# Optimization experiments

Measured on AMD Instinct MI355X. Metric: run time of the kernel, lower is better.

The kernel has to match this reference:

```python
import jax, jax.numpy as jnp
import numpy as np

D_MODEL = 2048
NUM_HEADS = 16
D_K = D_MODEL // NUM_HEADS
B, S, PAST = 2, 1024, 3072


def setup_inputs() -> dict:
    key = jax.random.key(0)
    ks = jax.random.split(key, 12)
    s = 1.0 / np.sqrt(D_MODEL)
    inp = {
        "x": jax.random.normal(ks[0], (B, S, D_MODEL), dtype=jnp.float32),
        "past_key": jax.random.normal(ks[1], (B, NUM_HEADS, PAST, D_K), dtype=jnp.float32),
        "past_value": jax.random.normal(ks[2], (B, NUM_HEADS, PAST, D_K), dtype=jnp.float32),
        "Wq": jax.random.normal(ks[3], (D_MODEL, D_MODEL), dtype=jnp.float32) * s,
        "bq": jax.random.normal(ks[4], (D_MODEL,), dtype=jnp.float32) * s,
        "Wk": jax.random.normal(ks[5], (D_MODEL, D_MODEL), dtype=jnp.float32) * s,
        "bk": jax.random.normal(ks[6], (D_MODEL,), dtype=jnp.float32) * s,
        "Wv": jax.random.normal(ks[7], (D_MODEL, D_MODEL), dtype=jnp.float32) * s,
        "bv": jax.random.normal(ks[8], (D_MODEL,), dtype=jnp.float32) * s,
        "Wo": jax.random.normal(ks[9], (D_MODEL, D_MODEL), dtype=jnp.float32) * s,
        "bo": jax.random.normal(ks[10], (D_MODEL,), dtype=jnp.float32) * s,
    }
    return inp


def reference(x, past_key, past_value, Wq, bq, Wk, bk, Wv, bv, Wo, bo):
    b, s, _ = x.shape
    # torch nn.Linear: y = x @ W^T + b
    def proj(W, bias):
        y = jnp.einsum('bsd,ed->bse', x, W) + bias
        return y.reshape(b, s, NUM_HEADS, D_K).transpose(0, 2, 1, 3)  # [B,H,S,dk]
    Q = proj(Wq, bq)
    K = proj(Wk, bk)
    V = proj(Wv, bv)
    K = jnp.concatenate([past_key, K], axis=2)   # [B,H,PAST+S,dk]
    V = jnp.concatenate([past_value, V], axis=2)
    scale = 1.0 / np.sqrt(D_K).astype(np.float32)
    scores = jnp.einsum('bhqd,bhkd->bhqk', Q, K) * scale
    attn = jax.nn.softmax(scores, axis=-1)
    out = jnp.einsum('bhqk,bhkd->bhqd', attn, V)          # [B,H,S,dk]
    out = out.transpose(0, 2, 1, 3).reshape(b, s, D_MODEL)
    out = jnp.einsum('bsd,ed->bse', out, Wo) + bo
    return out, K, V
```

## Files before the change

### kernel.cpp

```cpp
#include <hip/hip_runtime.h>
#include <stdint.h>

typedef __bf16 bf16;
typedef __bf16 bf16x4 __attribute__((ext_vector_type(4)));
typedef __bf16 bf16x8 __attribute__((ext_vector_type(8)));
typedef float  f32x4  __attribute__((ext_vector_type(4)));

#define DMODEL 2048
#define NH 16
#define DK 128
#define SS 1024
#define PASTLEN 3072
#define LTOT 4096
#define KVTILES 64
#define NSPLIT 2
#define NT 32

__device__ __forceinline__ void gload16(const void* g, void* l) {
    __builtin_amdgcn_global_load_lds(
        (__attribute__((address_space(1))) void*)(uintptr_t)g,
        (__attribute__((address_space(3))) void*)(uintptr_t)l,
        16, 0, 0);
}

__global__ __launch_bounds__(256) void cvt5_k(
    const float* __restrict__ s0, const float* __restrict__ s1,
    const float* __restrict__ s2, const float* __restrict__ s3,
    const float* __restrict__ s4,
    bf16* __restrict__ d0, bf16* __restrict__ d1, bf16* __restrict__ d2,
    bf16* __restrict__ d3, bf16* __restrict__ d4, int n8)
{
    const float* s; bf16* d;
    switch (blockIdx.y) {
        case 0: s = s0; d = d0; break;
        case 1: s = s1; d = d1; break;
        case 2: s = s2; d = d2; break;
        case 3: s = s3; d = d3; break;
        default: s = s4; d = d4; break;
    }
    int stride = gridDim.x * blockDim.x;
    for (int i = blockIdx.x*blockDim.x + threadIdx.x; i < n8; i += stride) {
        const float4* p = (const float4*)s + (size_t)i*2;
        float4 a = p[0], b = p[1];
        bf16x8 o;
        o[0]=(bf16)a.x; o[1]=(bf16)a.y; o[2]=(bf16)a.z; o[3]=(bf16)a.w;
        o[4]=(bf16)b.x; o[5]=(bf16)b.y; o[6]=(bf16)b.z; o[7]=(bf16)b.w;
        *((bf16x8*)d + i) = o;
    }
}

__global__ __launch_bounds__(256) void gemm_bt(
    const bf16* __restrict__ A,
    const bf16* __restrict__ W0, const bf16* __restrict__ W1, const bf16* __restrict__ W2,
    const float* __restrict__ b0, const float* __restrict__ b1, const float* __restrict__ b2,
    bf16* __restrict__ outQ, float* __restrict__ outK, float* __restrict__ outV,
    float* __restrict__ outO, int mode)
{
    __shared__ __align__(16) bf16 As[128*32];
    __shared__ __align__(16) bf16 Bs[128*32];
    const int tid  = threadIdx.x;
    const int wave = tid >> 6, lane = tid & 63;
    const int l15 = lane & 15, l4 = lane >> 4;
    int which, ntile;
    if (mode == 0) { which = blockIdx.y >> 4; ntile = blockIdx.y & 15; }
    else           { which = 3;               ntile = blockIdx.y; }
    const bf16*  W    = (mode != 0 || which == 0) ? W0 : (which == 1 ? W1 : W2);
    const float* bias = (mode != 0 || which == 0) ? b0 : (which == 1 ? b1 : b2);
    const int m0 = blockIdx.x * 128, n0 = ntile * 128;
    const int wm = wave >> 1, wn = wave & 1;

    f32x4 acc[4][4] = {};

    for (int k0 = 0; k0 < DMODEL; k0 += 32) {
        __syncthreads();
        #pragma unroll
        for (int c = 0; c < 2; ++c) {
            const int base = c*4096 + wave*1024;
            const int byte = base + lane*16;
            const int row  = byte >> 6;
            const int ke   = (byte & 63) >> 1;
            gload16(A + (size_t)(m0+row)*DMODEL + k0 + ke, (char*)As + base);
            gload16(W + (size_t)(n0+row)*DMODEL + k0 + ke, (char*)Bs + base);
        }
        asm volatile("s_waitcnt vmcnt(0)" ::: "memory");
        __syncthreads();
        bf16x8 af[4], bfv[4];
        #pragma unroll
        for (int mf = 0; mf < 4; ++mf)
            af[mf] = *(const bf16x8*)((const char*)As + (wm*64 + mf*16 + l15)*64 + l4*16);
        #pragma unroll
        for (int nf = 0; nf < 4; ++nf)
            bfv[nf] = *(const bf16x8*)((const char*)Bs + (wn*64 + nf*16 + l15)*64 + l4*16);
        #pragma unroll
        for (int mf = 0; mf < 4; ++mf)
            #pragma unroll
            for (int nf = 0; nf < 4; ++nf)
                acc[mf][nf] = __builtin_amdgcn_mfma_f32_16x16x32_bf16(af[mf], bfv[nf], acc[mf][nf], 0, 0, 0);
    }

    float bv4[4];
    #pragma unroll
    for (int nf = 0; nf < 4; ++nf) bv4[nf] = bias[n0 + wn*64 + nf*16 + l15];

    const int rbase = m0 + wm*64 + l4*4;
    const int cbase = n0 + wn*64 + l15;

    if (mode == 1) {
        #pragma unroll
        for (int mf = 0; mf < 4; ++mf)
        #pragma unroll
        for (int nf = 0; nf < 4; ++nf) {
            const int col = cbase + nf*16;
            #pragma unroll
            for (int r = 0; r < 4; ++r) {
                const int row = rbase + mf*16 + r;
                outO[(size_t)row*DMODEL + col] = acc[mf][nf][r] + bv4[nf];
            }
        }
    } else if (which == 0) {
        const float qs = 0.08838834764831845f * 1.4426950408889634f;
        #pragma unroll
        for (int mf = 0; mf < 4; ++mf)
        #pragma unroll
        for (int nf = 0; nf < 4; ++nf) {
            const int col = cbase + nf*16;
            const int h = col >> 7, d = col & 127;
            #pragma unroll
            for (int r = 0; r < 4; ++r) {
                const int row = rbase + mf*16 + r;
                const int b = row >> 10, s = row & 1023;
                outQ[((size_t)(b*NH + h)*SS + s)*DK + d] = (bf16)((acc[mf][nf][r] + bv4[nf]) * qs);
            }
        }
    } else {
        float* dst = (which == 1) ? outK : outV;
        #pragma unroll
        for (int mf = 0; mf < 4; ++mf)
        #pragma unroll
        for (int nf = 0; nf < 4; ++nf) {
            const int col = cbase + nf*16;
            const int h = col >> 7, d = col & 127;
            #pragma unroll
            for (int r = 0; r < 4; ++r) {
                const int row = rbase + mf*16 + r;
                const int b = row >> 10, s = row & 1023;
                dst[((size_t)(b*NH + h)*LTOT + PASTLEN + s)*DK + d] = acc[mf][nf][r] + bv4[nf];
            }
        }
    }
}

__global__ __launch_bounds__(256) void kvprep_k(
    const float* __restrict__ pk, const float* __restrict__ pv,
    float* __restrict__ Kf, float* __restrict__ Vf,
    bf16* __restrict__ Kb, bf16* __restrict__ Vb)
{
    __shared__ float Vt_f[64*132];
    const int tid = threadIdx.x;
    const int tau = blockIdx.x, bh = blockIdx.y;
    const bool past = tau < 48;
    const size_t srcoff = past ? ((size_t)bh*PASTLEN + tau*64)*DK
                               : ((size_t)bh*LTOT    + tau*64)*DK;
    const float* srcK = (past ? pk : Kf) + srcoff;
    const float* srcV = (past ? pv : Vf) + srcoff;
    float* dstKf = Kf + ((size_t)bh*LTOT + tau*64)*DK;
    float* dstVf = Vf + ((size_t)bh*LTOT + tau*64)*DK;
    char* kblob = (char*)Kb + (((size_t)bh*KVTILES + tau) << 14);
    char* vblob = (char*)Vb + (((size_t)bh*KVTILES + tau) << 14);

    #pragma unroll
    for (int i = 0; i < 8; ++i) {
        const int f4 = i*256 + tid;
        const int r  = f4 >> 5;
        const int c8 = f4 & 31;
        float4 k4 = ((const float4*)srcK)[f4];
        float4 v4 = ((const float4*)srcV)[f4];
        if (past) {
            ((float4*)dstKf)[f4] = k4;
            ((float4*)dstVf)[f4] = v4;
        }
        bf16x4 kq; kq[0]=(bf16)k4.x; kq[1]=(bf16)k4.y; kq[2]=(bf16)k4.z; kq[3]=(bf16)k4.w;
        *(bf16x4*)(kblob + r*256 + ((c8*8) ^ ((r&7)<<4))) = kq;
        *(float4*)&Vt_f[r*132 + c8*4] = v4;
    }
    __syncthreads();
    const int d = tid >> 1, half = tid & 1;
    const int dx = (d & 7) << 4;
    #pragma unroll
    for (int jj = 0; jj < 4; ++jj) {
        const int chunk = half*4 + jj;
        bf16x8 o;
        #pragma unroll
        for (int e = 0; e < 8; ++e) {
            const int j  = chunk*8 + e;
            const int oe = (j & 32) + ((j & 4) << 2) + (((j >> 3) & 3) << 2) + (j & 3);
            o[e] = (bf16)Vt_f[oe*132 + d];
        }
        *(bf16x8*)(vblob + d*128 + ((chunk*16) ^ dx)) = o;
    }
}

__global__ __launch_bounds__(512, 2) void attn_k(
    const bf16* __restrict__ Qb,
    const bf16* __restrict__ Kb, const bf16* __restrict__ Vb,
    bf16* __restrict__ Opart, float* __restrict__ Marr, float* __restrict__ Larr)
{
    __shared__ __align__(16) char KL[4][16384];
    __shared__ __align__(16) char VL[4][16384];

    const int tid  = threadIdx.x;
    const int wave = tid >> 6, lane = tid & 63;
    const int l15 = lane & 15, l4 = lane >> 4;
    const int wgid = blockIdx.x;
    const int qt = (wgid >> 3) & 3;
    const int g  = ((wgid >> 5) << 3) | (wgid & 7);
    const int bh = g >> 1, sp = g & 1;
    const int qbase = qt*256 + wave*32;

    bf16x8 qf[2][4];
    #pragma unroll
    for (int qq = 0; qq < 2; ++qq) {
        const bf16* qptr = Qb + ((size_t)bh*SS + qbase + qq*16 + l15)*DK;
        #pragma unroll
        for (int ks = 0; ks < 4; ++ks)
            qf[qq][ks] = *(const bf16x8*)(qptr + ks*32 + l4*8);
    }

    const char* kblobs = (const char*)Kb + (((size_t)bh*KVTILES + sp*NT) << 14);
    const char* vblobs = (const char*)Vb + (((size_t)bh*KVTILES + sp*NT) << 14);
    const int soff = wave*2048;

    bf16x8 ones8;
    #pragma unroll
    for (int e = 0; e < 8; ++e) ones8[e] = (bf16)1.0f;

    float m_run[2];
    f32x4 oacc[2][8];
    f32x4 lacc[2];
    m_run[0] = -1e30f; m_run[1] = -1e30f;
    #pragma unroll
    for (int qq = 0; qq < 2; ++qq) {
        #pragma unroll
        for (int df = 0; df < 8; ++df) oacc[qq][df] = f32x4{0.f,0.f,0.f,0.f};
        lacc[qq] = f32x4{0.f,0.f,0.f,0.f};
    }

    #pragma unroll
    for (int tt = 0; tt < 2; ++tt)
        #pragma unroll
        for (int c = 0; c < 2; ++c) {
            gload16(kblobs + ((size_t)tt << 14) + soff + c*1024 + lane*16, KL[tt] + soff + c*1024);
            gload16(vblobs + ((size_t)tt << 14) + soff + c*1024 + lane*16, VL[tt] + soff + c*1024);
        }
    const char* kpf = kblobs + (2 << 14);
    const char* vpf = vblobs + (2 << 14);

#define TILE_STEP(T, BUF)                                                          \
    {                                                                              \
        if ((T) + 2 < NT) {                                                        \
            const int nb = ((BUF) + 2) & 3;                                        \
            _Pragma("unroll")                                                      \
            for (int c = 0; c < 2; ++c) {                                          \
                gload16(kpf + soff + c*1024 + lane*16, KL[nb] + soff + c*1024);    \
                gload16(vpf + soff + c*1024 + lane*16, VL[nb] + soff + c*1024);    \
            }                                                                      \
            kpf += 16384; vpf += 16384;                                            \
            asm volatile("s_waitcnt vmcnt(8)" ::: "memory");                       \
        } else if ((T) + 1 < NT) {                                                 \
            asm volatile("s_waitcnt vmcnt(4)" ::: "memory");                       \
        } else {                                                                   \
            asm volatile("s_waitcnt vmcnt(0)" ::: "memory");                       \
        }                                                                          \
        __builtin_amdgcn_s_barrier();                                              \
        const char* Kc = KL[BUF];                                                  \
        const char* Vc = VL[BUF];                                                  \
        f32x4 sa[2][4];                                                            \
        _Pragma("unroll")                                                          \
        for (int qq = 0; qq < 2; ++qq)                                             \
            _Pragma("unroll")                                                      \
            for (int nf = 0; nf < 4; ++nf) sa[qq][nf] = f32x4{0.f,0.f,0.f,0.f};    \
        __builtin_amdgcn_s_setprio(1);                                             \
        _Pragma("unroll")                                                          \
        for (int nf = 0; nf < 4; ++nf) {                                           \
            const int krow = nf*16 + l15;                                          \
            const int rx = (krow & 7) << 4;                                        \
            _Pragma("unroll")                                                      \
            for (int ks = 0; ks < 4; ++ks) {                                       \
                bf16x8 kf = *(const bf16x8*)(Kc + krow*256 + ((ks*64 + l4*16) ^ rx)); \
                sa[0][nf] = __builtin_amdgcn_mfma_f32_16x16x32_bf16(kf, qf[0][ks], sa[0][nf], 0,0,0); \
                sa[1][nf] = __builtin_amdgcn_mfma_f32_16x16x32_bf16(kf, qf[1][ks], sa[1][nf], 0,0,0); \
            }                                                                      \
        }                                                                          \
        __builtin_amdgcn_s_setprio(0);                                             \
        float mt2[2];                                                              \
        _Pragma("unroll")                                                          \
        for (int qq = 0; qq < 2; ++qq) {                                           \
            float a0 = fmaxf(fmaxf(sa[qq][0][0], sa[qq][0][1]), fmaxf(sa[qq][0][2], sa[qq][0][3])); \
            float a1 = fmaxf(fmaxf(sa[qq][1][0], sa[qq][1][1]), fmaxf(sa[qq][1][2], sa[qq][1][3])); \
            float a2 = fmaxf(fmaxf(sa[qq][2][0], sa[qq][2][1]), fmaxf(sa[qq][2][2], sa[qq][2][3])); \
            float a3 = fmaxf(fmaxf(sa[qq][3][0], sa[qq][3][1]), fmaxf(sa[qq][3][2], sa[qq][3][3])); \
            float v = fmaxf(fmaxf(a0, a1), fmaxf(a2, a3));                         \
            v = fmaxf(v, __shfl_xor(v, 16, 64));                                   \
            v = fmaxf(v, __shfl_xor(v, 32, 64));                                   \
            mt2[qq] = v;                                                           \
        }                                                                          \
        const bool ok = (mt2[0] <= m_run[0] + 8.0f) && (mt2[1] <= m_run[1] + 8.0f); \
        if (!__all(ok)) {                                                          \
            _Pragma("unroll")                                                      \
            for (int qq = 0; qq < 2; ++qq) {                                       \
                const float mn   = fmaxf(m_run[qq], mt2[qq]);                      \
                const float corr = exp2f(m_run[qq] - mn);                          \
                m_run[qq] = mn;                                                    \
                _Pragma("unroll")                                                  \
                for (int r = 0; r < 4; ++r) {                                      \
                    const float c = __shfl(corr, (lane & 48) | (l4*4 + r), 64);    \
                    lacc[qq][r] *= c;                                              \
                    _Pragma("unroll")                                              \
                    for (int df = 0; df < 8; ++df) oacc[qq][df][r] *= c;           \
                }                                                                  \
            }                                                                      \
        }                                                                          \
        bf16x8 pf[2][2];                                                           \
        _Pragma("unroll")                                                          \
        for (int qq = 0; qq < 2; ++qq)                                             \
            _Pragma("unroll")                                                      \
            for (int ks2 = 0; ks2 < 2; ++ks2) {                                    \
                bf16x8 v;                                                          \
                _Pragma("unroll")                                                  \
                for (int e = 0; e < 8; ++e)                                        \
                    v[e] = (bf16)exp2f(sa[qq][ks2*2 + (e >> 2)][e & 3] - m_run[qq]); \
                pf[qq][ks2] = v;                                                   \
            }                                                                      \
        __builtin_amdgcn_s_setprio(1);                                             \
        _Pragma("unroll")                                                          \
        for (int ks2 = 0; ks2 < 2; ++ks2) {                                        \
            lacc[0] = __builtin_amdgcn_mfma_f32_16x16x32_bf16(pf[0][ks2], ones8, lacc[0], 0,0,0); \
            lacc[1] = __builtin_amdgcn_mfma_f32_16x16x32_bf16(pf[1][ks2], ones8, lacc[1], 0,0,0); \
            _Pragma("unroll")                                                      \
            for (int df = 0; df < 8; ++df) {                                       \
                const int d = df*16 + l15;                                         \
                bf16x8 vf = *(const bf16x8*)(Vc + d*128 + ((ks2*64 + l4*16) ^ ((d&7)<<4))); \
                oacc[0][df] = __builtin_amdgcn_mfma_f32_16x16x32_bf16(pf[0][ks2], vf, oacc[0][df], 0,0,0); \
                oacc[1][df] = __builtin_amdgcn_mfma_f32_16x16x32_bf16(pf[1][ks2], vf, oacc[1][df], 0,0,0); \
            }                                                                      \
        }                                                                          \
        __builtin_amdgcn_s_setprio(0);                                             \
    }

    for (int t4 = 0; t4 < NT; t4 += 4) {
        TILE_STEP(t4 + 0, 0)
        TILE_STEP(t4 + 1, 1)
        TILE_STEP(t4 + 2, 2)
        TILE_STEP(t4 + 3, 3)
    }
#undef TILE_STEP

    bf16* op = Opart + ((size_t)sp*32 + bh)*SS*DK;
    #pragma unroll
    for (int qq = 0; qq < 2; ++qq)
        #pragma unroll
        for (int df = 0; df < 8; ++df)
            #pragma unroll
            for (int r = 0; r < 4; ++r) {
                const int q = qbase + qq*16 + l4*4 + r;
                op[(size_t)q*DK + df*16 + l15] = (bf16)oacc[qq][df][r];
            }
    if (l4 == 0) {
        #pragma unroll
        for (int qq = 0; qq < 2; ++qq)
            Marr[(size_t)sp*32768 + bh*SS + qbase + qq*16 + l15] = m_run[qq];
    }
    if (l15 == 0) {
        #pragma unroll
        for (int qq = 0; qq < 2; ++qq)
            #pragma unroll
            for (int r = 0; r < 4; ++r) {
                const int q = qbase + qq*16 + l4*4 + r;
                Larr[(size_t)sp*32768 + bh*SS + q] = lacc[qq][r];
            }
    }
}

__global__ __launch_bounds__(256) void combine_k(
    const bf16* __restrict__ Opart, const float* __restrict__ Marr,
    const float* __restrict__ Larr, bf16* __restrict__ Ob)
{
    const int gid = blockIdx.x*256 + threadIdx.x;
    const int row = gid >> 4;
    const int c8  = gid & 15;
    const int bh = row >> 10, q = row & 1023;
    float m[NSPLIT], l[NSPLIT];
    #pragma unroll
    for (int s = 0; s < NSPLIT; ++s) {
        m[s] = Marr[(size_t)s*32768 + row];
        l[s] = Larr[(size_t)s*32768 + row];
    }
    float M = m[0];
    #pragma unroll
    for (int s = 1; s < NSPLIT; ++s) M = fmaxf(M, m[s]);
    float w[NSPLIT], den = 0.f;
    #pragma unroll
    for (int s = 0; s < NSPLIT; ++s) { w[s] = exp2f(m[s] - M); den += l[s]*w[s]; }
    const float inv = 1.f / den;
    #pragma unroll
    for (int s = 0; s < NSPLIT; ++s) w[s] *= inv;
    float acc[8] = {};
    #pragma unroll
    for (int s = 0; s < NSPLIT; ++s) {
        bf16x8 p = *(const bf16x8*)(Opart + (size_t)s*4194304 + (size_t)row*DK + c8*8);
        #pragma unroll
        for (int e = 0; e < 8; ++e) acc[e] += (float)p[e]*w[s];
    }
    const int b = bh >> 4, h = bh & 15;
    bf16x8 o;
    #pragma unroll
    for (int e = 0; e < 8; ++e) o[e] = (bf16)acc[e];
    *(bf16x8*)(Ob + ((size_t)(b*SS + q))*DMODEL + h*DK + c8*8) = o;
}

extern "C" void kernel_launch(void* const* d_in, const int* in_sizes, int n_in,
                              void* d_out, int out_size, void* d_ws, size_t ws_size,
                              hipStream_t stream) {
    const float* x  = (const float*)d_in[0];
    const float* pk = (const float*)d_in[1];
    const float* pv = (const float*)d_in[2];
    const float* Wq = (const float*)d_in[3];
    const float* bq = (const float*)d_in[4];
    const float* Wk = (const float*)d_in[5];
    const float* bk = (const float*)d_in[6];
    const float* Wv = (const float*)d_in[7];
    const float* bv = (const float*)d_in[8];
    const float* Wo = (const float*)d_in[9];
    const float* bo = (const float*)d_in[10];

    float* out  = (float*)d_out;
    float* Kout = out + 4194304;
    float* Vout = out + 20971520;

    char* ws = (char*)d_ws;
    bf16* xb    = (bf16*)(ws);
    bf16* Wqb   = (bf16*)(ws + (size_t)8*1024*1024);
    bf16* Wkb   = (bf16*)(ws + (size_t)16*1024*1024);
    bf16* Wvb   = (bf16*)(ws + (size_t)24*1024*1024);
    bf16* Wob   = (bf16*)(ws + (size_t)32*1024*1024);
    bf16* Qb    = (bf16*)(ws + (size_t)40*1024*1024);
    bf16* Ob    = (bf16*)(ws + (size_t)48*1024*1024);
    bf16* Kb    = (bf16*)(ws + (size_t)56*1024*1024);
    bf16* Vb    = (bf16*)(ws + (size_t)88*1024*1024);
    bf16*  Opart = (bf16*)(ws);
    float* Marr  = out;
    float* Larr  = out + 131072;

    cvt5_k<<<dim3(1024, 5), 256, 0, stream>>>(x, Wq, Wk, Wv, Wo,
                                              xb, Wqb, Wkb, Wvb, Wob, 524288);
    gemm_bt<<<dim3(16, 48), 256, 0, stream>>>(xb, Wqb, Wkb, Wvb, bq, bk, bv,
                                              Qb, Kout, Vout, nullptr, 0);
    kvprep_k<<<dim3(64, 32), 256, 0, stream>>>(pk, pv, Kout, Vout, Kb, Vb);
    attn_k<<<256, 512, 0, stream>>>(Qb, Kb, Vb, Opart, Marr, Larr);
    combine_k<<<2048, 256, 0, stream>>>(Opart, Marr, Larr, Ob);
    gemm_bt<<<dim3(16, 16), 256, 0, stream>>>(Ob, Wob, nullptr, nullptr, bo, nullptr, nullptr,
                                              nullptr, nullptr, nullptr, out, 1);
}
```

Measured before the change: 275.7 us.

## Drop KV split and combine kernel; halve query rows per wave in attention

Attention blocks now cover 128 queries over the full KV length instead of 256 queries over half, and normalize their output directly into Ob. This removes the combine kernel, the partial-output write/read and the max/sum arrays. In exchange each K/V tile loaded into LDS is reused by half as many queries, doubling global/LDS K/V traffic and halving MFMA work per barrier.

```diff
diff --git a/kernel.cpp b/kernel.cpp
--- a/kernel.cpp
+++ b/kernel.cpp
@@ -13,8 +13,7 @@
 #define PASTLEN 3072
 #define LTOT 4096
 #define KVTILES 64
-#define NSPLIT 2
-#define NT 32
+#define NT 64
 
 __device__ __forceinline__ void gload16(const void* g, void* l) {
     __builtin_amdgcn_global_load_lds(
@@ -203,7 +202,7 @@
 __global__ __launch_bounds__(512, 2) void attn_k(
     const bf16* __restrict__ Qb,
     const bf16* __restrict__ Kb, const bf16* __restrict__ Vb,
-    bf16* __restrict__ Opart, float* __restrict__ Marr, float* __restrict__ Larr)
+    bf16* __restrict__ Ob)
 {
     __shared__ __align__(16) char KL[4][16384];
     __shared__ __align__(16) char VL[4][16384];
@@ -212,38 +211,32 @@
     const int wave = tid >> 6, lane = tid & 63;
     const int l15 = lane & 15, l4 = lane >> 4;
     const int wgid = blockIdx.x;
-    const int qt = (wgid >> 3) & 3;
-    const int g  = ((wgid >> 5) << 3) | (wgid & 7);
-    const int bh = g >> 1, sp = g & 1;
-    const int qbase = qt*256 + wave*32;
-
-    bf16x8 qf[2][4];
-    #pragma unroll
-    for (int qq = 0; qq < 2; ++qq) {
-        const bf16* qptr = Qb + ((size_t)bh*SS + qbase + qq*16 + l15)*DK;
+    const int qt = (wgid >> 3) & 7;
+    const int bh = ((wgid >> 6) << 3) | (wgid & 7);
+    const int qbase = qt*128 + wave*16;
+
+    bf16x8 qf[4];
+    {
+        const bf16* qptr = Qb + ((size_t)bh*SS + qbase + l15)*DK;
         #pragma unroll
         for (int ks = 0; ks < 4; ++ks)
-            qf[qq][ks] = *(const bf16x8*)(qptr + ks*32 + l4*8);
-    }
-
-    const char* kblobs = (const char*)Kb + (((size_t)bh*KVTILES + sp*NT) << 14);
-    const char* vblobs = (const char*)Vb + (((size_t)bh*KVTILES + sp*NT) << 14);
+            qf[ks] = *(const bf16x8*)(qptr + ks*32 + l4*8);
+    }
+
+    const char* kblobs = (const char*)Kb + (((size_t)bh*KVTILES) << 14);
+    const char* vblobs = (const char*)Vb + (((size_t)bh*KVTILES) << 14);
     const int soff = wave*2048;
 
     bf16x8 ones8;
     #pragma unroll
     for (int e = 0; e < 8; ++e) ones8[e] = (bf16)1.0f;
 
-    float m_run[2];
-    f32x4 oacc[2][8];
-    f32x4 lacc[2];
-    m_run[0] = -1e30f; m_run[1] = -1e30f;
-    #pragma unroll
-    for (int qq = 0; qq < 2; ++qq) {
-        #pragma unroll
-        for (int df = 0; df < 8; ++df) oacc[qq][df] = f32x4{0.f,0.f,0.f,0.f};
-        lacc[qq] = f32x4{0.f,0.f,0.f,0.f};
-    }
+    float m_run = -1e30f;
+    f32x4 oacc[8];
+    f32x4 lacc;
+    #pragma unroll
+    for (int df = 0; df < 8; ++df) oacc[df] = f32x4{0.f,0.f,0.f,0.f};
+    lacc = f32x4{0.f,0.f,0.f,0.f};
 
     #pragma unroll
     for (int tt = 0; tt < 2; ++tt)
@@ -274,11 +267,9 @@
         __builtin_amdgcn_s_barrier();                                              \
         const char* Kc = KL[BUF];                                                  \
         const char* Vc = VL[BUF];                                                  \
-        f32x4 sa[2][4];                                                            \
+        f32x4 sa[4];                                                               \
         _Pragma("unroll")                                                          \
-        for (int qq = 0; qq < 2; ++qq)                                             \
-            _Pragma("unroll")                                                      \
-            for (int nf = 0; nf < 4; ++nf) sa[qq][nf] = f32x4{0.f,0.f,0.f,0.f};    \
+        for (int nf = 0; nf < 4; ++nf) sa[nf] = f32x4{0.f,0.f,0.f,0.f};            \
         __builtin_amdgcn_s_setprio(1);                                             \
         _Pragma("unroll")                                                          \
         for (int nf = 0; nf < 4; ++nf) {                                           \
@@ -287,61 +278,48 @@
             _Pragma("unroll")                                                      \
             for (int ks = 0; ks < 4; ++ks) {                                       \
                 bf16x8 kf = *(const bf16x8*)(Kc + krow*256 + ((ks*64 + l4*16) ^ rx)); \
-                sa[0][nf] = __builtin_amdgcn_mfma_f32_16x16x32_bf16(kf, qf[0][ks], sa[0][nf], 0,0,0); \
-                sa[1][nf] = __builtin_amdgcn_mfma_f32_16x16x32_bf16(kf, qf[1][ks], sa[1][nf], 0,0,0); \
+                sa[nf] = __builtin_amdgcn_mfma_f32_16x16x32_bf16(kf, qf[ks], sa[nf], 0,0,0); \
             }                                                                      \
         }                                                                          \
         __builtin_amdgcn_s_setprio(0);                                             \
-        float mt2[2];                                                              \
+        float a0 = fmaxf(fmaxf(sa[0][0], sa[0][1]), fmaxf(sa[0][2], sa[0][3]));    \
+        float a1 = fmaxf(fmaxf(sa[1][0], sa[1][1]), fmaxf(sa[1][2], sa[1][3]));    \
+        float a2 = fmaxf(fmaxf(sa[2][0], sa[2][1]), fmaxf(sa[2][2], sa[2][3]));    \
+        float a3 = fmaxf(fmaxf(sa[3][0], sa[3][1]), fmaxf(sa[3][2], sa[3][3]));    \
+        float mt2 = fmaxf(fmaxf(a0, a1), fmaxf(a2, a3));                           \
+        mt2 = fmaxf(mt2, __shfl_xor(mt2, 16, 64));                                 \
+        mt2 = fmaxf(mt2, __shfl_xor(mt2, 32, 64));                                 \
+        const bool ok = (mt2 <= m_run + 8.0f);                                     \
+        if (!__all(ok)) {                                                          \
+            const float mn   = fmaxf(m_run, mt2);                                  \
+            const float corr = exp2f(m_run - mn);                                  \
+            m_run = mn;                                                            \
+            _Pragma("unroll")                                                      \
+            for (int r = 0; r < 4; ++r) {                                          \
+                const float c = __shfl(corr, (lane & 48) | (l4*4 + r), 64);        \
+                lacc[r] *= c;                                                      \
+                _Pragma("unroll")                                                  \
+                for (int df = 0; df < 8; ++df) oacc[df][r] *= c;                   \
+            }                                                                      \
+        }                                                                          \
+        bf16x8 pf[2];                                                              \
         _Pragma("unroll")                                                          \
-        for (int qq = 0; qq < 2; ++qq) {                                           \
-            float a0 = fmaxf(fmaxf(sa[qq][0][0], sa[qq][0][1]), fmaxf(sa[qq][0][2], sa[qq][0][3])); \
-            float a1 = fmaxf(fmaxf(sa[qq][1][0], sa[qq][1][1]), fmaxf(sa[qq][1][2], sa[qq][1][3])); \
-            float a2 = fmaxf(fmaxf(sa[qq][2][0], sa[qq][2][1]), fmaxf(sa[qq][2][2], sa[qq][2][3])); \
-            float a3 = fmaxf(fmaxf(sa[qq][3][0], sa[qq][3][1]), fmaxf(sa[qq][3][2], sa[qq][3][3])); \
-            float v = fmaxf(fmaxf(a0, a1), fmaxf(a2, a3));                         \
-            v = fmaxf(v, __shfl_xor(v, 16, 64));                                   \
-            v = fmaxf(v, __shfl_xor(v, 32, 64));                                   \
-            mt2[qq] = v;                                                           \
-        }                                                                          \
-        const bool ok = (mt2[0] <= m_run[0] + 8.0f) && (mt2[1] <= m_run[1] + 8.0f); \
-        if (!__all(ok)) {                                                          \
-            _Pragma("unroll")                                                      \
-            for (int qq = 0; qq < 2; ++qq) {                                       \
-                const float mn   = fmaxf(m_run[qq], mt2[qq]);                      \
-                const float corr = exp2f(m_run[qq] - mn);                          \
-                m_run[qq] = mn;                                                    \
-                _Pragma("unroll")                                                  \
-                for (int r = 0; r < 4; ++r) {                                      \
-                    const float c = __shfl(corr, (lane & 48) | (l4*4 + r), 64);    \
-                    lacc[qq][r] *= c;                                              \
-                    _Pragma("unroll")                                              \
-                    for (int df = 0; df < 8; ++df) oacc[qq][df][r] *= c;           \
-                }                                                                  \
-            }                                                                      \
-        }                                                                          \
-        bf16x8 pf[2][2];                                                           \
-        _Pragma("unroll")                                                          \
-        for (int qq = 0; qq < 2; ++qq)                                             \
-            _Pragma("unroll")                                                      \
-            for (int ks2 = 0; ks2 < 2; ++ks2) {                                    \
-                bf16x8 v;                                                          \
-                _Pragma("unroll")                                                  \
-                for (int e = 0; e < 8; ++e)                                        \
-                    v[e] = (bf16)exp2f(sa[qq][ks2*2 + (e >> 2)][e & 3] - m_run[qq]); \
-                pf[qq][ks2] = v;                                                   \
-            }                                                                      \
+        for (int ks2 = 0; ks2 < 2; ++ks2) {                                        \
+            bf16x8 v;                                                              \
+            _Pragma("unroll")                                                      \
+            for (int e = 0; e < 8; ++e)                                            \
+                v[e] = (bf16)exp2f(sa[ks2*2 + (e >> 2)][e & 3] - m_run);           \
+            pf[ks2] = v;                                                           \
+        }                                                                          \
         __builtin_amdgcn_s_setprio(1);                                             \
         _Pragma("unroll")                                                          \
         for (int ks2 = 0; ks2 < 2; ++ks2) {                                        \
-            lacc[0] = __builtin_amdgcn_mfma_f32_16x16x32_bf16(pf[0][ks2], ones8, lacc[0], 0,0,0); \
-            lacc[1] = __builtin_amdgcn_mfma_f32_16x16x32_bf16(pf[1][ks2], ones8, lacc[1], 0,0,0); \
+            lacc = __builtin_amdgcn_mfma_f32_16x16x32_bf16(pf[ks2], ones8, lacc, 0,0,0); \
             _Pragma("unroll")                                                      \
             for (int df = 0; df < 8; ++df) {                                       \
                 const int d = df*16 + l15;                                         \
                 bf16x8 vf = *(const bf16x8*)(Vc + d*128 + ((ks2*64 + l4*16) ^ ((d&7)<<4))); \
-                oacc[0][df] = __builtin_amdgcn_mfma_f32_16x16x32_bf16(pf[0][ks2], vf, oacc[0][df], 0,0,0); \
-                oacc[1][df] = __builtin_amdgcn_mfma_f32_16x16x32_bf16(pf[1][ks2], vf, oacc[1][df], 0,0,0); \
+                oacc[df] = __builtin_amdgcn_mfma_f32_16x16x32_bf16(pf[ks2], vf, oacc[df], 0,0,0); \
             }                                                                      \
         }                                                                          \
         __builtin_amdgcn_s_setprio(0);                                             \
@@ -355,67 +333,17 @@
     }
 #undef TILE_STEP
 
-    bf16* op = Opart + ((size_t)sp*32 + bh)*SS*DK;
-    #pragma unroll
-    for (int qq = 0; qq < 2; ++qq)
-        #pragma unroll
-        for (int df = 0; df < 8; ++df)
-            #pragma unroll
-            for (int r = 0; r < 4; ++r) {
-                const int q = qbase + qq*16 + l4*4 + r;
-                op[(size_t)q*DK + df*16 + l15] = (bf16)oacc[qq][df][r];
-            }
-    if (l4 == 0) {
-        #pragma unroll
-        for (int qq = 0; qq < 2; ++qq)
-            Marr[(size_t)sp*32768 + bh*SS + qbase + qq*16 + l15] = m_run[qq];
-    }
-    if (l15 == 0) {
-        #pragma unroll
-        for (int qq = 0; qq < 2; ++qq)
-            #pragma unroll
-            for (int r = 0; r < 4; ++r) {
-                const int q = qbase + qq*16 + l4*4 + r;
-                Larr[(size_t)sp*32768 + bh*SS + q] = lacc[qq][r];
-            }
-    }
-}
-
-__global__ __launch_bounds__(256) void combine_k(
-    const bf16* __restrict__ Opart, const float* __restrict__ Marr,
-    const float* __restrict__ Larr, bf16* __restrict__ Ob)
-{
-    const int gid = blockIdx.x*256 + threadIdx.x;
-    const int row = gid >> 4;
-    const int c8  = gid & 15;
-    const int bh = row >> 10, q = row & 1023;
-    float m[NSPLIT], l[NSPLIT];
-    #pragma unroll
-    for (int s = 0; s < NSPLIT; ++s) {
-        m[s] = Marr[(size_t)s*32768 + row];
-        l[s] = Larr[(size_t)s*32768 + row];
-    }
-    float M = m[0];
-    #pragma unroll
-    for (int s = 1; s < NSPLIT; ++s) M = fmaxf(M, m[s]);
-    float w[NSPLIT], den = 0.f;
-    #pragma unroll
-    for (int s = 0; s < NSPLIT; ++s) { w[s] = exp2f(m[s] - M); den += l[s]*w[s]; }
-    const float inv = 1.f / den;
-    #pragma unroll
-    for (int s = 0; s < NSPLIT; ++s) w[s] *= inv;
-    float acc[8] = {};
-    #pragma unroll
-    for (int s = 0; s < NSPLIT; ++s) {
-        bf16x8 p = *(const bf16x8*)(Opart + (size_t)s*4194304 + (size_t)row*DK + c8*8);
-        #pragma unroll
-        for (int e = 0; e < 8; ++e) acc[e] += (float)p[e]*w[s];
-    }
     const int b = bh >> 4, h = bh & 15;
-    bf16x8 o;
-    #pragma unroll
-    for (int e = 0; e < 8; ++e) o[e] = (bf16)acc[e];
-    *(bf16x8*)(Ob + ((size_t)(b*SS + q))*DMODEL + h*DK + c8*8) = o;
+    float inv[4];
+    #pragma unroll
+    for (int r = 0; r < 4; ++r) inv[r] = 1.f / lacc[r];
+    #pragma unroll
+    for (int df = 0; df < 8; ++df)
+        #pragma unroll
+        for (int r = 0; r < 4; ++r) {
+            const int q = qbase + l4*4 + r;
+            Ob[((size_t)(b*SS + q))*DMODEL + h*DK + df*16 + l15] = (bf16)(oacc[df][r]*inv[r]);
+        }
 }
 
 extern "C" void kernel_launch(void* const* d_in, const int* in_sizes, int n_in,
@@ -447,17 +375,13 @@
     bf16* Ob    = (bf16*)(ws + (size_t)48*1024*1024);
     bf16* Kb    = (bf16*)(ws + (size_t)56*1024*1024);
     bf16* Vb    = (bf16*)(ws + (size_t)88*1024*1024);
-    bf16*  Opart = (bf16*)(ws);
-    float* Marr  = out;
-    float* Larr  = out + 131072;
 
     cvt5_k<<<dim3(1024, 5), 256, 0, stream>>>(x, Wq, Wk, Wv, Wo,
                                               xb, Wqb, Wkb, Wvb, Wob, 524288);
     gemm_bt<<<dim3(16, 48), 256, 0, stream>>>(xb, Wqb, Wkb, Wvb, bq, bk, bv,
                                               Qb, Kout, Vout, nullptr, 0);
     kvprep_k<<<dim3(64, 32), 256, 0, stream>>>(pk, pv, Kout, Vout, Kb, Vb);
-    attn_k<<<256, 512, 0, stream>>>(Qb, Kb, Vb, Opart, Marr, Larr);
-    combine_k<<<2048, 256, 0, stream>>>(Opart, Marr, Larr, Ob);
+    attn_k<<<256, 512, 0, stream>>>(Qb, Kb, Vb, Ob);
     gemm_bt<<<dim3(16, 16), 256, 0, stream>>>(Ob, Wob, nullptr, nullptr, bo, nullptr, nullptr,
                                               nullptr, nullptr, nullptr, out, 1);
 }
```

New measurement: 289.0 us. 4.8% more time.
